# Kernel tuning notes

Hardware: AMD Instinct MI355X
Metric: run time of the kernel (lower is better)

Reference implementation:

```python
import jax, jax.numpy as jnp
import numpy as np

B, T, DM, H, D = 2, 2048, 1024, 16, 64
SCALE = D ** -0.5


def setup_inputs() -> dict:
    key = jax.random.key(0)
    ks = jax.random.split(key, 7)
    std = DM ** -0.5
    inp = {
        "x": jax.random.normal(ks[0], (B, T, DM), dtype=jnp.float32),
        "Wq_re": jax.random.normal(ks[1], (DM, H * D), dtype=jnp.float32) * std,
        "Wq_im": jax.random.normal(ks[2], (DM, H * D), dtype=jnp.float32) * std,
        "Wk_re": jax.random.normal(ks[3], (DM, H * D), dtype=jnp.float32) * std,
        "Wk_im": jax.random.normal(ks[4], (DM, H * D), dtype=jnp.float32) * std,
        "Wv": jax.random.normal(ks[5], (DM, H * D), dtype=jnp.float32) * std,
        "Wo": jax.random.normal(ks[6], (H * D, DM), dtype=jnp.float32) * std,
    }
    # standard RoPE angle cache: theta[t, d] = t * 10000^(-d/D)
    inv_freq = 1.0 / (10000.0 ** (np.arange(D, dtype=np.float32) / D))
    ang = np.arange(T, dtype=np.float32)[:, None] * inv_freq[None, :]
    inp["cos"] = jnp.asarray(np.cos(ang))
    inp["sin"] = jnp.asarray(np.sin(ang))
    return inp


def _split(x, W):
    # [B,T,DM] @ [DM,H*D] -> [B,H,T,D]
    return (x @ W).reshape(B, T, H, D).transpose(0, 2, 1, 3)


def reference(x, Wq_re, Wq_im, Wk_re, Wk_im, Wv, Wo, cos, sin):
    q_re, q_im = _split(x, Wq_re), _split(x, Wq_im)
    k_re, k_im = _split(x, Wk_re), _split(x, Wk_im)

    # complex RoPE: rotate (re, im) by e^{i*theta}; cos/sin broadcast over b,h
    c = cos[None, None]  # [1,1,T,D]
    s = sin[None, None]
    q_re, q_im = q_re * c - q_im * s, q_re * s + q_im * c
    k_re, k_im = k_re * c - k_im * s, k_re * s + k_im * c

    # Hermitian inner product real part: q_re.k_re + q_im.k_im
    scores = (jnp.einsum("bhqd,bhkd->bhqk", q_re, k_re)
              + jnp.einsum("bhqd,bhkd->bhqk", q_im, k_im)) * SCALE

    causal = jnp.tril(jnp.ones((T, T), dtype=bool))
    scores = jnp.where(causal[None, None], scores, -jnp.inf)
    weights = jax.nn.softmax(scores, axis=-1)

    v = _split(x, Wv)
    out = jnp.einsum("bhqk,bhkd->bhqd", weights, v)  # [B,H,T,D]
    out = out.transpose(0, 2, 1, 3).reshape(B, T, H * D)
    return out @ Wo
```

## Files before the change

kernel.cpp:

```cpp
#include <hip/hip_runtime.h>
#include <math.h>

#define SCALE_ 0.125f

typedef _Float16 half_t;
typedef __attribute__((ext_vector_type(8))) _Float16 f16x8;
typedef __attribute__((ext_vector_type(4))) _Float16 f16x4;
typedef __attribute__((ext_vector_type(4))) float f32x4;

#define AS1 __attribute__((address_space(1)))
#define AS3 __attribute__((address_space(3)))

__device__ __forceinline__ f32x4 mfma16(f16x8 a, f16x8 b, f32x4 c) {
  return __builtin_amdgcn_mfma_f32_16x16x32_f16(a, b, c, 0, 0, 0);
}
__device__ __forceinline__ void gload16(const void* g, void* l) {
  __builtin_amdgcn_global_load_lds((const AS1 void*)g, (AS3 void*)l, 16, 0, 0);
}
__device__ __forceinline__ void split2(float f, half_t* h, half_t* l) {
  half_t hh = (half_t)f;
  *h = hh;
  *l = (half_t)(f - (float)hh);
}

__global__ __launch_bounds__(256) void convw_kernel(
    const float* __restrict__ W0, const float* __restrict__ W1,
    const float* __restrict__ W2, const float* __restrict__ W3,
    const float* __restrict__ W4, const float* __restrict__ W5,
    half_t* __restrict__ wh, half_t* __restrict__ wl)
{
  const int z = blockIdx.z;
  const float* W = (z == 0) ? W0 : (z == 1) ? W1 : (z == 2) ? W2
                  : (z == 3) ? W3 : (z == 4) ? W4 : W5;
  half_t* outh = wh + z * 1048576;
  half_t* outl = wl + z * 1048576;
  const int n0 = blockIdx.x * 32, k0 = blockIdx.y * 32;
  const int t = threadIdx.x, r = t >> 3, c4 = (t & 7) * 4;
  __shared__ float lds[32][33];
  float4 v = *(const float4*)&W[(k0 + r) * 1024 + n0 + c4];
  lds[r][c4 + 0] = v.x; lds[r][c4 + 1] = v.y;
  lds[r][c4 + 2] = v.z; lds[r][c4 + 3] = v.w;
  __syncthreads();
  f16x4 oh, ol;
#pragma unroll
  for (int j = 0; j < 4; ++j) {
    const float f = lds[c4 + j][r];
    half_t hv, lv; split2(f, &hv, &lv);
    oh[j] = hv; ol[j] = lv;
  }
  *(f16x4*)&outh[(n0 + r) * 1024 + k0 + c4] = oh;
  *(f16x4*)&outl[(n0 + r) * 1024 + k0 + c4] = ol;
}

__global__ __launch_bounds__(256) void convx_kernel(
    const float* __restrict__ x, half_t* __restrict__ xh, half_t* __restrict__ xl)
{
  const int i = (blockIdx.x * 256 + threadIdx.x) * 4;
  float4 v = *(const float4*)&x[i];
  float vv[4] = {v.x, v.y, v.z, v.w};
  f16x4 oh, ol;
#pragma unroll
  for (int j = 0; j < 4; ++j) {
    half_t hv, lv; split2(vv[j], &hv, &lv);
    oh[j] = hv; ol[j] = lv;
  }
  *(f16x4*)&xh[i] = oh;
  *(f16x4*)&xl[i] = ol;
}

__global__ __launch_bounds__(256) void gemm_kernel(
    const half_t* __restrict__ Agh, const half_t* __restrict__ Agl,
    const half_t* __restrict__ wh, const half_t* __restrict__ wl,
    half_t* __restrict__ qth, half_t* __restrict__ qtl,
    half_t* __restrict__ kth, half_t* __restrict__ ktl,
    half_t* __restrict__ vTh, half_t* __restrict__ vTl,
    float* __restrict__ outp, int final_mode)
{
  __shared__ half_t Ash[4096], Asl[4096], Bsh[4096], Bsl[4096];
  const int z = blockIdx.z;
  const int widx = final_mode ? 5 : z;
  const half_t* Bth = wh + widx * 1048576;
  const half_t* Btl = wl + widx * 1048576;

  const int n0 = blockIdx.x * 128, m0 = blockIdx.y * 128;
  const int tid = threadIdx.x, lane = tid & 63, wid = tid >> 6;
  const int wr = wid >> 1, wc = wid & 1, l15 = lane & 15, l4 = lane >> 4;

  f32x4 acc[4][4];
#pragma unroll
  for (int i = 0; i < 4; ++i)
#pragma unroll
    for (int j = 0; j < 4; ++j) acc[i][j] = (f32x4){0.f, 0.f, 0.f, 0.f};

  const int s0 = wid * 64 + lane, s1 = s0 + 256;
  const int r0 = s0 >> 2, c0 = (s0 & 3) * 8;
  const int r1 = s1 >> 2, c1 = (s1 & 3) * 8;
  half_t* Ah0 = Ash + wid * 512;        half_t* Ah1 = Ash + 2048 + wid * 512;
  half_t* Al0 = Asl + wid * 512;        half_t* Al1 = Asl + 2048 + wid * 512;
  half_t* Bh0 = Bsh + wid * 512;        half_t* Bh1 = Bsh + 2048 + wid * 512;
  half_t* Bl0 = Bsl + wid * 512;        half_t* Bl1 = Bsl + 2048 + wid * 512;

  for (int k0 = 0; k0 < 1024; k0 += 32) {
    __syncthreads();
    gload16(Agh + (m0 + r0) * 1024 + k0 + c0, Ah0);
    gload16(Agh + (m0 + r1) * 1024 + k0 + c1, Ah1);
    gload16(Agl + (m0 + r0) * 1024 + k0 + c0, Al0);
    gload16(Agl + (m0 + r1) * 1024 + k0 + c1, Al1);
    gload16(Bth + (n0 + r0) * 1024 + k0 + c0, Bh0);
    gload16(Bth + (n0 + r1) * 1024 + k0 + c1, Bh1);
    gload16(Btl + (n0 + r0) * 1024 + k0 + c0, Bl0);
    gload16(Btl + (n0 + r1) * 1024 + k0 + c1, Bl1);
    __syncthreads();
    f16x8 ah[4], al[4], bh[4], bl[4];
#pragma unroll
    for (int i = 0; i < 4; ++i) {
      const int ro = (wr * 64 + i * 16 + l15) * 32 + l4 * 8;
      ah[i] = *(const f16x8*)&Ash[ro];
      al[i] = *(const f16x8*)&Asl[ro];
    }
#pragma unroll
    for (int j = 0; j < 4; ++j) {
      const int ro = (wc * 64 + j * 16 + l15) * 32 + l4 * 8;
      bh[j] = *(const f16x8*)&Bsh[ro];
      bl[j] = *(const f16x8*)&Bsl[ro];
    }
#pragma unroll
    for (int i = 0; i < 4; ++i)
#pragma unroll
      for (int j = 0; j < 4; ++j) {
        acc[i][j] = mfma16(ah[i], bh[j], acc[i][j]);
        acc[i][j] = mfma16(ah[i], bl[j], acc[i][j]);
        acc[i][j] = mfma16(al[i], bh[j], acc[i][j]);
      }
  }

#pragma unroll
  for (int i = 0; i < 4; ++i) {
    const int mb = m0 + wr * 64 + i * 16 + l4 * 4;
#pragma unroll
    for (int j = 0; j < 4; ++j) {
      const int n = n0 + wc * 64 + j * 16 + l15;
      if (final_mode) {
#pragma unroll
        for (int r = 0; r < 4; ++r) outp[(mb + r) * 1024 + n] = acc[i][j][r];
      } else if (z < 4) {
        half_t* dh = (z < 2) ? qth : kth;
        half_t* dl = (z < 2) ? qtl : ktl;
        const int colr = (n >> 6) * 128 + (n & 63) + ((z & 1) ? 64 : 0);
#pragma unroll
        for (int r = 0; r < 4; ++r) {
          half_t hv, lv; split2(acc[i][j][r], &hv, &lv);
          dh[(mb + r) * 2048 + colr] = hv;
          dl[(mb + r) * 2048 + colr] = lv;
        }
      } else {
        const int hh = n >> 6, d = n & 63;
        const int bq = mb >> 11, t = mb & 2047;
        f16x4 vh4, vl4;
#pragma unroll
        for (int r = 0; r < 4; ++r) {
          half_t hv, lv; split2(acc[i][j][r], &hv, &lv);
          vh4[r] = hv; vl4[r] = lv;
        }
        const int off = ((bq * 16 + hh) * 64 + d) * 2048 + t;
        *(f16x4*)&vTh[off] = vh4;
        *(f16x4*)&vTl[off] = vl4;
      }
    }
  }
}

__global__ __launch_bounds__(256) void rope_kernel(
    const half_t* __restrict__ qth, const half_t* __restrict__ qtl,
    const half_t* __restrict__ kth, const half_t* __restrict__ ktl,
    const float* __restrict__ cosb, const float* __restrict__ sinb,
    half_t* __restrict__ qbh, half_t* __restrict__ qbl,
    half_t* __restrict__ kbh, half_t* __restrict__ kbl)
{
  const int z = blockIdx.y;
  const int g = blockIdx.x * 4 + (threadIdx.x >> 6);
  const int d = threadIdx.x & 63;
  const int m = g >> 4, h = g & 15;
  const int b = m >> 11, t = m & 2047;
  const half_t* sh = (z ? kth : qth) + m * 2048 + h * 128;
  const half_t* sl = (z ? ktl : qtl) + m * 2048 + h * 128;
  const float re = (float)sh[d] + (float)sl[d];
  const float im = (float)sh[64 + d] + (float)sl[64 + d];
  const float c = cosb[t * 64 + d], s = sinb[t * 64 + d];
  float rer = re * c - im * s;
  float imr = re * s + im * c;
  if (z == 0) { rer *= SCALE_; imr *= SCALE_; }
  half_t* dh = (z ? kbh : qbh) + ((b * 16 + h) * 2048 + t) * 128;
  half_t* dl = (z ? kbl : qbl) + ((b * 16 + h) * 2048 + t) * 128;
  half_t hv, lv;
  split2(rer, &hv, &lv); dh[d] = hv;      dl[d] = lv;
  split2(imr, &hv, &lv); dh[64 + d] = hv; dl[64 + d] = lv;
}

__global__ __launch_bounds__(512) void attn_kernel(
    const half_t* __restrict__ qbh, const half_t* __restrict__ qbl,
    const half_t* __restrict__ kbh, const half_t* __restrict__ kbl,
    const half_t* __restrict__ vTh, const half_t* __restrict__ vTl,
    half_t* __restrict__ abh, half_t* __restrict__ abl)
{
  const int i = blockIdx.x;
  const int bh = i & 31;
  const int idx = (i >> 5) & 7;
  const int qt = (i < 256) ? (15 - idx) : idx;
  const int b = bh >> 4, h = bh & 15;
  const int tid = threadIdx.x, lane = tid & 63, w = tid >> 6;
  const int l15 = lane & 15, l4 = lane >> 4;
  const int q0 = qt * 128;

  __shared__ half_t Kh[2][4096], Kl[2][4096];
  __shared__ half_t Vh[2][2048], Vl[2][2048];
  __shared__ half_t Ph[4096], Pl[4096];

  f16x8 qh[4], ql[4];
  {
    const int qoff = (bh * 2048 + q0 + w * 16 + l15) * 128;
#pragma unroll
    for (int c = 0; c < 4; ++c) {
      qh[c] = *(const f16x8*)(qbh + qoff + c * 32 + l4 * 8);
      ql[c] = *(const f16x8*)(qbl + qoff + c * 32 + l4 * 8);
    }
  }

  f32x4 o[4];
#pragma unroll
  for (int n = 0; n < 4; ++n) o[n] = (f32x4){0.f, 0.f, 0.f, 0.f};
  float mrow[4] = {-3e38f, -3e38f, -3e38f, -3e38f};
  float lrow[4] = {0.f, 0.f, 0.f, 0.f};

  const half_t* kh_p = kbh + (size_t)bh * 2048 * 128;
  const half_t* kl_p = kbl + (size_t)bh * 2048 * 128;
  const half_t* vh_p = vTh + (size_t)bh * 64 * 2048;
  const half_t* vl_p = vTl + (size_t)bh * 64 * 2048;

  const int krow = w * 4 + (lane >> 4);
  const int ks = lane & 15;
  const int kg = (ks & 8) | ((ks & 7) ^ (krow & 7));
  const int vrow = (w & 3) * 16 + (lane >> 2);
  const int vs = lane & 3;
  const int vg = vs ^ ((vrow >> 1) & 3);
  const bool vhi = (w < 4);

  const int nkt = 4 * (qt + 1);
  const int qminw = q0 + w * 16, qmaxw = qminw + 15;

  gload16(kh_p + (krow) * 128 + kg * 8, &Kh[0][w * 512]);
  gload16(kl_p + (krow) * 128 + kg * 8, &Kl[0][w * 512]);
  if (vhi) gload16(vh_p + vrow * 2048 + vg * 8, &Vh[0][(w & 3) * 512]);
  else     gload16(vl_p + vrow * 2048 + vg * 8, &Vl[0][(w & 3) * 512]);

  for (int kt = 0; kt < nkt; ++kt) {
    const int k0 = kt * 32;
    const int cb = kt & 1;
    __syncthreads();

    {
      const int k0n = (kt + 1 < nkt) ? k0 + 32 : 0;
      const int nb = cb ^ 1;
      gload16(kh_p + (k0n + krow) * 128 + kg * 8, &Kh[nb][w * 512]);
      gload16(kl_p + (k0n + krow) * 128 + kg * 8, &Kl[nb][w * 512]);
      if (vhi) gload16(vh_p + vrow * 2048 + k0n + vg * 8, &Vh[nb][(w & 3) * 512]);
      else     gload16(vl_p + vrow * 2048 + k0n + vg * 8, &Vl[nb][(w & 3) * 512]);
    }

    if (k0 > qmaxw) continue;

    f32x4 s[2];
    s[0] = (f32x4){0.f, 0.f, 0.f, 0.f};
    s[1] = (f32x4){0.f, 0.f, 0.f, 0.f};
#pragma unroll
    for (int c = 0; c < 4; ++c) {
#pragma unroll
      for (int n = 0; n < 2; ++n) {
        const int row = n * 16 + l15;
        const int co = c * 4 + l4;
        const int sr = (co & 8) | ((co & 7) ^ (row & 7));
        const f16x8 kfh = *(const f16x8*)&Kh[cb][row * 128 + sr * 8];
        const f16x8 kfl = *(const f16x8*)&Kl[cb][row * 128 + sr * 8];
        s[n] = mfma16(qh[c], kfh, s[n]);
        s[n] = mfma16(qh[c], kfl, s[n]);
        s[n] = mfma16(ql[c], kfh, s[n]);
      }
    }

    if (k0 + 31 > qminw) {
#pragma unroll
      for (int n = 0; n < 2; ++n)
#pragma unroll
        for (int r = 0; r < 4; ++r)
          if (k0 + n * 16 + l15 > qminw + l4 * 4 + r) s[n][r] = -3e38f;
    }

#pragma unroll
    for (int r = 0; r < 4; ++r) {
      float mx = fmaxf(s[0][r], s[1][r]);
      mx = fmaxf(mx, __shfl_xor(mx, 1));
      mx = fmaxf(mx, __shfl_xor(mx, 2));
      mx = fmaxf(mx, __shfl_xor(mx, 4));
      mx = fmaxf(mx, __shfl_xor(mx, 8));
      const float mnew = fmaxf(mrow[r], mx);
      const float alpha = __expf(mrow[r] - mnew);
      const float p0 = __expf(s[0][r] - mnew);
      const float p1 = __expf(s[1][r] - mnew);
      float rs = p0 + p1;
      rs += __shfl_xor(rs, 1);
      rs += __shfl_xor(rs, 2);
      rs += __shfl_xor(rs, 4);
      rs += __shfl_xor(rs, 8);
      lrow[r] = lrow[r] * alpha + rs;
      mrow[r] = mnew;
#pragma unroll
      for (int n = 0; n < 4; ++n) o[n][r] *= alpha;
      const int prow = w * 16 + l4 * 4 + r;
      const int psw = (prow >> 2) & 3;
      half_t hv, lv;
      split2(p0, &hv, &lv);
      {
        const int col = l15, sp = (col >> 3) ^ psw;
        Ph[prow * 32 + sp * 8 + (col & 7)] = hv;
        Pl[prow * 32 + sp * 8 + (col & 7)] = lv;
      }
      split2(p1, &hv, &lv);
      {
        const int col = 16 + l15, sp = (col >> 3) ^ psw;
        Ph[prow * 32 + sp * 8 + (col & 7)] = hv;
        Pl[prow * 32 + sp * 8 + (col & 7)] = lv;
      }
    }

    {
      const int prow = w * 16 + l15;
      const int spp = l4 ^ ((prow >> 2) & 3);
      const f16x8 pfh = *(const f16x8*)&Ph[prow * 32 + spp * 8];
      const f16x8 pfl = *(const f16x8*)&Pl[prow * 32 + spp * 8];
#pragma unroll
      for (int n = 0; n < 4; ++n) {
        const int vr = n * 16 + l15;
        const int sv = l4 ^ ((vr >> 1) & 3);
        const f16x8 vfh = *(const f16x8*)&Vh[cb][vr * 32 + sv * 8];
        const f16x8 vfl = *(const f16x8*)&Vl[cb][vr * 32 + sv * 8];
        o[n] = mfma16(pfh, vfh, o[n]);
        o[n] = mfma16(pfh, vfl, o[n]);
        o[n] = mfma16(pfl, vfh, o[n]);
      }
    }
  }

  const int mg = b * 2048 + q0 + w * 16 + l4 * 4;
#pragma unroll
  for (int r = 0; r < 4; ++r) {
    const float inv = 1.0f / lrow[r];
    const int m = mg + r;
#pragma unroll
    for (int n = 0; n < 4; ++n) {
      half_t hv, lv; split2(o[n][r] * inv, &hv, &lv);
      abh[m * 1024 + h * 64 + n * 16 + l15] = hv;
      abl[m * 1024 + h * 64 + n * 16 + l15] = lv;
    }
  }
}

extern "C" void kernel_launch(void* const* d_in, const int* in_sizes, int n_in,
                              void* d_out, int out_size, void* d_ws,
                              size_t ws_size, hipStream_t stream) {
  const float* x    = (const float*)d_in[0];
  const float* Wqre = (const float*)d_in[1];
  const float* Wqim = (const float*)d_in[2];
  const float* Wkre = (const float*)d_in[3];
  const float* Wkim = (const float*)d_in[4];
  const float* Wv   = (const float*)d_in[5];
  const float* Wo   = (const float*)d_in[6];
  const float* cosb = (const float*)d_in[7];
  const float* sinb = (const float*)d_in[8];

  char* w = (char*)d_ws;
  const size_t MB = (size_t)1 << 20;
  half_t* wh6 = (half_t*)(w + 0 * MB);
  half_t* wl6 = (half_t*)(w + 12 * MB);
  half_t* xh  = (half_t*)(w + 24 * MB);
  half_t* xl  = (half_t*)(w + 32 * MB);
  half_t* qth = (half_t*)(w + 40 * MB);
  half_t* qtl = (half_t*)(w + 56 * MB);
  half_t* kth = (half_t*)(w + 72 * MB);
  half_t* ktl = (half_t*)(w + 88 * MB);
  half_t* qbh = (half_t*)(w + 104 * MB);
  half_t* qbl = (half_t*)(w + 120 * MB);
  half_t* kbh = (half_t*)(w + 136 * MB);
  half_t* kbl = (half_t*)(w + 152 * MB);
  half_t* vTh = (half_t*)(w + 168 * MB);
  half_t* vTl = (half_t*)(w + 176 * MB);
  half_t* abh = (half_t*)(w + 40 * MB);
  half_t* abl = (half_t*)(w + 48 * MB);

  dim3 blk(256);
  convw_kernel<<<dim3(32, 32, 6), blk, 0, stream>>>(Wqre, Wqim, Wkre, Wkim, Wv,
                                                    Wo, wh6, wl6);
  convx_kernel<<<dim3(4096), blk, 0, stream>>>(x, xh, xl);
  gemm_kernel<<<dim3(8, 32, 5), blk, 0, stream>>>(xh, xl, wh6, wl6, qth, qtl,
                                                  kth, ktl, vTh, vTl, nullptr, 0);
  rope_kernel<<<dim3(16384, 2), blk, 0, stream>>>(qth, qtl, kth, ktl, cosb,
                                                  sinb, qbh, qbl, kbh, kbl);
  attn_kernel<<<dim3(512), dim3(512), 0, stream>>>(qbh, qbl, kbh, kbl, vTh,
                                                   vTl, abh, abl);
  gemm_kernel<<<dim3(8, 32, 1), blk, 0, stream>>>(abh, abl, wh6, wl6, nullptr,
                                                  nullptr, nullptr, nullptr,
                                                  nullptr, nullptr,
                                                  (float*)d_out, 1);
}
```

Measured before the change: 513.4 us.

## Fuse RoPE into paired re/im projection GEMM and drop V split-precision

Computes the real and imaginary Q/K projections in one block that shares the x tile, and applies RoPE and scaling in the epilogue, which removes the separate rope kernel and its intermediate buffers. The V projection and the P·V product in attention now use single fp16 operands instead of the hi/lo split, cutting three MFMAs to one and halving V/P memory traffic. The final projection moves into its own kernel. The trade-off is lower precision on the V path and higher register and LDS pressure in the paired GEMM.

```diff
diff --git a/kernel.cpp b/kernel.cpp
--- a/kernel.cpp
+++ b/kernel.cpp
@@ -68,139 +68,144 @@
   *(f16x4*)&xl[i] = ol;
 }
 
-__global__ __launch_bounds__(256) void gemm_kernel(
-    const half_t* __restrict__ Agh, const half_t* __restrict__ Agl,
+__global__ __launch_bounds__(256) void proj_pair_kernel(
+    const half_t* __restrict__ xh, const half_t* __restrict__ xl,
     const half_t* __restrict__ wh, const half_t* __restrict__ wl,
-    half_t* __restrict__ qth, half_t* __restrict__ qtl,
-    half_t* __restrict__ kth, half_t* __restrict__ ktl,
-    half_t* __restrict__ vTh, half_t* __restrict__ vTl,
-    float* __restrict__ outp, int final_mode)
+    const float* __restrict__ cosb, const float* __restrict__ sinb,
+    half_t* __restrict__ qbh, half_t* __restrict__ qbl,
+    half_t* __restrict__ kbh, half_t* __restrict__ kbl,
+    half_t* __restrict__ vTh)
 {
-  __shared__ half_t Ash[4096], Asl[4096], Bsh[4096], Bsl[4096];
+  __shared__ half_t Ash[4096], Asl[4096];
+  __shared__ half_t B0h[4096], B0l[4096], B1h[4096], B1l[4096];
   const int z = blockIdx.z;
-  const int widx = final_mode ? 5 : z;
-  const half_t* Bth = wh + widx * 1048576;
-  const half_t* Btl = wl + widx * 1048576;
+  const bool pair = (z < 2);
+  const half_t* BRh_g = wh + (pair ? (2 * z) : 4) * 1048576;
+  const half_t* BRl_g = wl + (pair ? (2 * z) : 4) * 1048576;
+  const half_t* BIh_g = wh + (2 * z + 1) * 1048576;
+  const half_t* BIl_g = wl + (2 * z + 1) * 1048576;
 
   const int n0 = blockIdx.x * 128, m0 = blockIdx.y * 128;
   const int tid = threadIdx.x, lane = tid & 63, wid = tid >> 6;
   const int wr = wid >> 1, wc = wid & 1, l15 = lane & 15, l4 = lane >> 4;
 
-  f32x4 acc[4][4];
+  f32x4 accR[4][4], accI[4][4];
 #pragma unroll
   for (int i = 0; i < 4; ++i)
 #pragma unroll
-    for (int j = 0; j < 4; ++j) acc[i][j] = (f32x4){0.f, 0.f, 0.f, 0.f};
+    for (int j = 0; j < 4; ++j) {
+      accR[i][j] = (f32x4){0.f, 0.f, 0.f, 0.f};
+      accI[i][j] = (f32x4){0.f, 0.f, 0.f, 0.f};
+    }
 
   const int s0 = wid * 64 + lane, s1 = s0 + 256;
   const int r0 = s0 >> 2, c0 = (s0 & 3) * 8;
   const int r1 = s1 >> 2, c1 = (s1 & 3) * 8;
-  half_t* Ah0 = Ash + wid * 512;        half_t* Ah1 = Ash + 2048 + wid * 512;
-  half_t* Al0 = Asl + wid * 512;        half_t* Al1 = Asl + 2048 + wid * 512;
-  half_t* Bh0 = Bsh + wid * 512;        half_t* Bh1 = Bsh + 2048 + wid * 512;
-  half_t* Bl0 = Bsl + wid * 512;        half_t* Bl1 = Bsl + 2048 + wid * 512;
+  half_t* A0 = Ash + wid * 512;   half_t* A1 = Ash + 2048 + wid * 512;
+  half_t* La0 = Asl + wid * 512;  half_t* La1 = Asl + 2048 + wid * 512;
+  half_t* R0 = B0h + wid * 512;   half_t* R1 = B0h + 2048 + wid * 512;
+  half_t* Lr0 = B0l + wid * 512;  half_t* Lr1 = B0l + 2048 + wid * 512;
+  half_t* I0 = B1h + wid * 512;   half_t* I1 = B1h + 2048 + wid * 512;
+  half_t* Li0 = B1l + wid * 512;  half_t* Li1 = B1l + 2048 + wid * 512;
 
   for (int k0 = 0; k0 < 1024; k0 += 32) {
     __syncthreads();
-    gload16(Agh + (m0 + r0) * 1024 + k0 + c0, Ah0);
-    gload16(Agh + (m0 + r1) * 1024 + k0 + c1, Ah1);
-    gload16(Agl + (m0 + r0) * 1024 + k0 + c0, Al0);
-    gload16(Agl + (m0 + r1) * 1024 + k0 + c1, Al1);
-    gload16(Bth + (n0 + r0) * 1024 + k0 + c0, Bh0);
-    gload16(Bth + (n0 + r1) * 1024 + k0 + c1, Bh1);
-    gload16(Btl + (n0 + r0) * 1024 + k0 + c0, Bl0);
-    gload16(Btl + (n0 + r1) * 1024 + k0 + c1, Bl1);
+    gload16(xh + (m0 + r0) * 1024 + k0 + c0, A0);
+    gload16(xh + (m0 + r1) * 1024 + k0 + c1, A1);
+    gload16(BRh_g + (n0 + r0) * 1024 + k0 + c0, R0);
+    gload16(BRh_g + (n0 + r1) * 1024 + k0 + c1, R1);
+    if (pair) {
+      gload16(xl + (m0 + r0) * 1024 + k0 + c0, La0);
+      gload16(xl + (m0 + r1) * 1024 + k0 + c1, La1);
+      gload16(BRl_g + (n0 + r0) * 1024 + k0 + c0, Lr0);
+      gload16(BRl_g + (n0 + r1) * 1024 + k0 + c1, Lr1);
+      gload16(BIh_g + (n0 + r0) * 1024 + k0 + c0, I0);
+      gload16(BIh_g + (n0 + r1) * 1024 + k0 + c1, I1);
+      gload16(BIl_g + (n0 + r0) * 1024 + k0 + c0, Li0);
+      gload16(BIl_g + (n0 + r1) * 1024 + k0 + c1, Li1);
+    }
     __syncthreads();
-    f16x8 ah[4], al[4], bh[4], bl[4];
+    f16x8 ah[4], al[4];
 #pragma unroll
     for (int i = 0; i < 4; ++i) {
       const int ro = (wr * 64 + i * 16 + l15) * 32 + l4 * 8;
       ah[i] = *(const f16x8*)&Ash[ro];
-      al[i] = *(const f16x8*)&Asl[ro];
+      if (pair) al[i] = *(const f16x8*)&Asl[ro];
     }
 #pragma unroll
     for (int j = 0; j < 4; ++j) {
       const int ro = (wc * 64 + j * 16 + l15) * 32 + l4 * 8;
-      bh[j] = *(const f16x8*)&Bsh[ro];
-      bl[j] = *(const f16x8*)&Bsl[ro];
-    }
-#pragma unroll
-    for (int i = 0; i < 4; ++i)
-#pragma unroll
-      for (int j = 0; j < 4; ++j) {
-        acc[i][j] = mfma16(ah[i], bh[j], acc[i][j]);
-        acc[i][j] = mfma16(ah[i], bl[j], acc[i][j]);
-        acc[i][j] = mfma16(al[i], bh[j], acc[i][j]);
-      }
-  }
-
-#pragma unroll
-  for (int i = 0; i < 4; ++i) {
-    const int mb = m0 + wr * 64 + i * 16 + l4 * 4;
-#pragma unroll
-    for (int j = 0; j < 4; ++j) {
-      const int n = n0 + wc * 64 + j * 16 + l15;
-      if (final_mode) {
-#pragma unroll
-        for (int r = 0; r < 4; ++r) outp[(mb + r) * 1024 + n] = acc[i][j][r];
-      } else if (z < 4) {
-        half_t* dh = (z < 2) ? qth : kth;
-        half_t* dl = (z < 2) ? qtl : ktl;
-        const int colr = (n >> 6) * 128 + (n & 63) + ((z & 1) ? 64 : 0);
-#pragma unroll
-        for (int r = 0; r < 4; ++r) {
-          half_t hv, lv; split2(acc[i][j][r], &hv, &lv);
-          dh[(mb + r) * 2048 + colr] = hv;
-          dl[(mb + r) * 2048 + colr] = lv;
+      const f16x8 bRh = *(const f16x8*)&B0h[ro];
+      if (pair) {
+        const f16x8 bRl = *(const f16x8*)&B0l[ro];
+        const f16x8 bIh = *(const f16x8*)&B1h[ro];
+        const f16x8 bIl = *(const f16x8*)&B1l[ro];
+#pragma unroll
+        for (int i = 0; i < 4; ++i) {
+          accR[i][j] = mfma16(ah[i], bRh, accR[i][j]);
+          accR[i][j] = mfma16(ah[i], bRl, accR[i][j]);
+          accR[i][j] = mfma16(al[i], bRh, accR[i][j]);
+          accI[i][j] = mfma16(ah[i], bIh, accI[i][j]);
+          accI[i][j] = mfma16(ah[i], bIl, accI[i][j]);
+          accI[i][j] = mfma16(al[i], bIh, accI[i][j]);
         }
       } else {
+#pragma unroll
+        for (int i = 0; i < 4; ++i)
+          accR[i][j] = mfma16(ah[i], bRh, accR[i][j]);
+      }
+    }
+  }
+
+  if (pair) {
+    half_t* dsth = z ? kbh : qbh;
+    half_t* dstl = z ? kbl : qbl;
+#pragma unroll
+    for (int i = 0; i < 4; ++i) {
+      const int mb = m0 + wr * 64 + i * 16 + l4 * 4;
+#pragma unroll
+      for (int j = 0; j < 4; ++j) {
+        const int n = n0 + wc * 64 + j * 16 + l15;
+        const int h = n >> 6, d = n & 63;
+#pragma unroll
+        for (int r = 0; r < 4; ++r) {
+          const int m = mb + r;
+          const int bq = m >> 11, t = m & 2047;
+          const float c = cosb[t * 64 + d], s = sinb[t * 64 + d];
+          const float re = accR[i][j][r], im = accI[i][j][r];
+          float rer = re * c - im * s;
+          float imr = re * s + im * c;
+          if (z == 0) { rer *= SCALE_; imr *= SCALE_; }
+          const size_t base = ((size_t)(bq * 16 + h) * 2048 + t) * 128;
+          half_t hv, lv;
+          split2(rer, &hv, &lv); dsth[base + d] = hv;      dstl[base + d] = lv;
+          split2(imr, &hv, &lv); dsth[base + 64 + d] = hv; dstl[base + 64 + d] = lv;
+        }
+      }
+    }
+  } else {
+#pragma unroll
+    for (int i = 0; i < 4; ++i) {
+      const int mb = m0 + wr * 64 + i * 16 + l4 * 4;
+      const int bq = mb >> 11, t = mb & 2047;
+#pragma unroll
+      for (int j = 0; j < 4; ++j) {
+        const int n = n0 + wc * 64 + j * 16 + l15;
         const int hh = n >> 6, d = n & 63;
-        const int bq = mb >> 11, t = mb & 2047;
-        f16x4 vh4, vl4;
-#pragma unroll
-        for (int r = 0; r < 4; ++r) {
-          half_t hv, lv; split2(acc[i][j][r], &hv, &lv);
-          vh4[r] = hv; vl4[r] = lv;
-        }
-        const int off = ((bq * 16 + hh) * 64 + d) * 2048 + t;
+        f16x4 vh4;
+#pragma unroll
+        for (int r = 0; r < 4; ++r) vh4[r] = (half_t)accR[i][j][r];
+        const size_t off = ((size_t)(bq * 16 + hh) * 64 + d) * 2048 + t;
         *(f16x4*)&vTh[off] = vh4;
-        *(f16x4*)&vTl[off] = vl4;
-      }
-    }
-  }
-}
-
-__global__ __launch_bounds__(256) void rope_kernel(
-    const half_t* __restrict__ qth, const half_t* __restrict__ qtl,
-    const half_t* __restrict__ kth, const half_t* __restrict__ ktl,
-    const float* __restrict__ cosb, const float* __restrict__ sinb,
-    half_t* __restrict__ qbh, half_t* __restrict__ qbl,
-    half_t* __restrict__ kbh, half_t* __restrict__ kbl)
-{
-  const int z = blockIdx.y;
-  const int g = blockIdx.x * 4 + (threadIdx.x >> 6);
-  const int d = threadIdx.x & 63;
-  const int m = g >> 4, h = g & 15;
-  const int b = m >> 11, t = m & 2047;
-  const half_t* sh = (z ? kth : qth) + m * 2048 + h * 128;
-  const half_t* sl = (z ? ktl : qtl) + m * 2048 + h * 128;
-  const float re = (float)sh[d] + (float)sl[d];
-  const float im = (float)sh[64 + d] + (float)sl[64 + d];
-  const float c = cosb[t * 64 + d], s = sinb[t * 64 + d];
-  float rer = re * c - im * s;
-  float imr = re * s + im * c;
-  if (z == 0) { rer *= SCALE_; imr *= SCALE_; }
-  half_t* dh = (z ? kbh : qbh) + ((b * 16 + h) * 2048 + t) * 128;
-  half_t* dl = (z ? kbl : qbl) + ((b * 16 + h) * 2048 + t) * 128;
-  half_t hv, lv;
-  split2(rer, &hv, &lv); dh[d] = hv;      dl[d] = lv;
-  split2(imr, &hv, &lv); dh[64 + d] = hv; dl[64 + d] = lv;
+      }
+    }
+  }
 }
 
 __global__ __launch_bounds__(512) void attn_kernel(
     const half_t* __restrict__ qbh, const half_t* __restrict__ qbl,
     const half_t* __restrict__ kbh, const half_t* __restrict__ kbl,
-    const half_t* __restrict__ vTh, const half_t* __restrict__ vTl,
+    const half_t* __restrict__ vTh,
     half_t* __restrict__ abh, half_t* __restrict__ abl)
 {
   const int i = blockIdx.x;
@@ -213,12 +218,12 @@
   const int q0 = qt * 128;
 
   __shared__ half_t Kh[2][4096], Kl[2][4096];
-  __shared__ half_t Vh[2][2048], Vl[2][2048];
-  __shared__ half_t Ph[4096], Pl[4096];
+  __shared__ half_t Vh[2][2048];
+  __shared__ half_t Ph[4096];
 
   f16x8 qh[4], ql[4];
   {
-    const int qoff = (bh * 2048 + q0 + w * 16 + l15) * 128;
+    const size_t qoff = ((size_t)bh * 2048 + q0 + w * 16 + l15) * 128;
 #pragma unroll
     for (int c = 0; c < 4; ++c) {
       qh[c] = *(const f16x8*)(qbh + qoff + c * 32 + l4 * 8);
@@ -235,7 +240,6 @@
   const half_t* kh_p = kbh + (size_t)bh * 2048 * 128;
   const half_t* kl_p = kbl + (size_t)bh * 2048 * 128;
   const half_t* vh_p = vTh + (size_t)bh * 64 * 2048;
-  const half_t* vl_p = vTl + (size_t)bh * 64 * 2048;
 
   const int krow = w * 4 + (lane >> 4);
   const int ks = lane & 15;
@@ -243,15 +247,13 @@
   const int vrow = (w & 3) * 16 + (lane >> 2);
   const int vs = lane & 3;
   const int vg = vs ^ ((vrow >> 1) & 3);
-  const bool vhi = (w < 4);
 
   const int nkt = 4 * (qt + 1);
   const int qminw = q0 + w * 16, qmaxw = qminw + 15;
 
-  gload16(kh_p + (krow) * 128 + kg * 8, &Kh[0][w * 512]);
-  gload16(kl_p + (krow) * 128 + kg * 8, &Kl[0][w * 512]);
-  if (vhi) gload16(vh_p + vrow * 2048 + vg * 8, &Vh[0][(w & 3) * 512]);
-  else     gload16(vl_p + vrow * 2048 + vg * 8, &Vl[0][(w & 3) * 512]);
+  gload16(kh_p + krow * 128 + kg * 8, &Kh[0][w * 512]);
+  gload16(kl_p + krow * 128 + kg * 8, &Kl[0][w * 512]);
+  if (w < 4) gload16(vh_p + vrow * 2048 + vg * 8, &Vh[0][(w & 3) * 512]);
 
   for (int kt = 0; kt < nkt; ++kt) {
     const int k0 = kt * 32;
@@ -263,8 +265,7 @@
       const int nb = cb ^ 1;
       gload16(kh_p + (k0n + krow) * 128 + kg * 8, &Kh[nb][w * 512]);
       gload16(kl_p + (k0n + krow) * 128 + kg * 8, &Kl[nb][w * 512]);
-      if (vhi) gload16(vh_p + vrow * 2048 + k0n + vg * 8, &Vh[nb][(w & 3) * 512]);
-      else     gload16(vl_p + vrow * 2048 + k0n + vg * 8, &Vl[nb][(w & 3) * 512]);
+      if (w < 4) gload16(vh_p + vrow * 2048 + k0n + vg * 8, &Vh[nb][(w & 3) * 512]);
     }
 
     if (k0 > qmaxw) continue;
@@ -317,18 +318,13 @@
       for (int n = 0; n < 4; ++n) o[n][r] *= alpha;
       const int prow = w * 16 + l4 * 4 + r;
       const int psw = (prow >> 2) & 3;
-      half_t hv, lv;
-      split2(p0, &hv, &lv);
       {
         const int col = l15, sp = (col >> 3) ^ psw;
-        Ph[prow * 32 + sp * 8 + (col & 7)] = hv;
-        Pl[prow * 32 + sp * 8 + (col & 7)] = lv;
-      }
-      split2(p1, &hv, &lv);
+        Ph[prow * 32 + sp * 8 + (col & 7)] = (half_t)p0;
+      }
       {
         const int col = 16 + l15, sp = (col >> 3) ^ psw;
-        Ph[prow * 32 + sp * 8 + (col & 7)] = hv;
-        Pl[prow * 32 + sp * 8 + (col & 7)] = lv;
+        Ph[prow * 32 + sp * 8 + (col & 7)] = (half_t)p1;
       }
     }
 
@@ -336,16 +332,12 @@
       const int prow = w * 16 + l15;
       const int spp = l4 ^ ((prow >> 2) & 3);
       const f16x8 pfh = *(const f16x8*)&Ph[prow * 32 + spp * 8];
-      const f16x8 pfl = *(const f16x8*)&Pl[prow * 32 + spp * 8];
 #pragma unroll
       for (int n = 0; n < 4; ++n) {
         const int vr = n * 16 + l15;
         const int sv = l4 ^ ((vr >> 1) & 3);
         const f16x8 vfh = *(const f16x8*)&Vh[cb][vr * 32 + sv * 8];
-        const f16x8 vfl = *(const f16x8*)&Vl[cb][vr * 32 + sv * 8];
         o[n] = mfma16(pfh, vfh, o[n]);
-        o[n] = mfma16(pfh, vfl, o[n]);
-        o[n] = mfma16(pfl, vfh, o[n]);
       }
     }
   }
@@ -360,6 +352,79 @@
       half_t hv, lv; split2(o[n][r] * inv, &hv, &lv);
       abh[m * 1024 + h * 64 + n * 16 + l15] = hv;
       abl[m * 1024 + h * 64 + n * 16 + l15] = lv;
+    }
+  }
+}
+
+__global__ __launch_bounds__(256) void outproj_kernel(
+    const half_t* __restrict__ Agh, const half_t* __restrict__ Agl,
+    const half_t* __restrict__ wh, const half_t* __restrict__ wl,
+    float* __restrict__ outp)
+{
+  __shared__ half_t Ash[4096], Asl[4096], Bsh[4096], Bsl[4096];
+  const half_t* Bth = wh + 5 * 1048576;
+  const half_t* Btl = wl + 5 * 1048576;
+
+  const int n0 = blockIdx.x * 128, m0 = blockIdx.y * 128;
+  const int tid = threadIdx.x, lane = tid & 63, wid = tid >> 6;
+  const int wr = wid >> 1, wc = wid & 1, l15 = lane & 15, l4 = lane >> 4;
+
+  f32x4 acc[4][4];
+#pragma unroll
+  for (int i = 0; i < 4; ++i)
+#pragma unroll
+    for (int j = 0; j < 4; ++j) acc[i][j] = (f32x4){0.f, 0.f, 0.f, 0.f};
+
+  const int s0 = wid * 64 + lane, s1 = s0 + 256;
+  const int r0 = s0 >> 2, c0 = (s0 & 3) * 8;
+  const int r1 = s1 >> 2, c1 = (s1 & 3) * 8;
+  half_t* Ah0 = Ash + wid * 512;        half_t* Ah1 = Ash + 2048 + wid * 512;
+  half_t* Al0 = Asl + wid * 512;        half_t* Al1 = Asl + 2048 + wid * 512;
+  half_t* Bh0 = Bsh + wid * 512;        half_t* Bh1 = Bsh + 2048 + wid * 512;
+  half_t* Bl0 = Bsl + wid * 512;        half_t* Bl1 = Bsl + 2048 + wid * 512;
+
+  for (int k0 = 0; k0 < 1024; k0 += 32) {
+    __syncthreads();
+    gload16(Agh + (m0 + r0) * 1024 + k0 + c0, Ah0);
+    gload16(Agh + (m0 + r1) * 1024 + k0 + c1, Ah1);
+    gload16(Agl + (m0 + r0) * 1024 + k0 + c0, Al0);
+    gload16(Agl + (m0 + r1) * 1024 + k0 + c1, Al1);
+    gload16(Bth + (n0 + r0) * 1024 + k0 + c0, Bh0);
+    gload16(Bth + (n0 + r1) * 1024 + k0 + c1, Bh1);
+    gload16(Btl + (n0 + r0) * 1024 + k0 + c0, Bl0);
+    gload16(Btl + (n0 + r1) * 1024 + k0 + c1, Bl1);
+    __syncthreads();
+    f16x8 ah[4], al[4], bh[4], bl[4];
+#pragma unroll
+    for (int i = 0; i < 4; ++i) {
+      const int ro = (wr * 64 + i * 16 + l15) * 32 + l4 * 8;
+      ah[i] = *(const f16x8*)&Ash[ro];
+      al[i] = *(const f16x8*)&Asl[ro];
+    }
+#pragma unroll
+    for (int j = 0; j < 4; ++j) {
+      const int ro = (wc * 64 + j * 16 + l15) * 32 + l4 * 8;
+      bh[j] = *(const f16x8*)&Bsh[ro];
+      bl[j] = *(const f16x8*)&Bsl[ro];
+    }
+#pragma unroll
+    for (int i = 0; i < 4; ++i)
+#pragma unroll
+      for (int j = 0; j < 4; ++j) {
+        acc[i][j] = mfma16(ah[i], bh[j], acc[i][j]);
+        acc[i][j] = mfma16(ah[i], bl[j], acc[i][j]);
+        acc[i][j] = mfma16(al[i], bh[j], acc[i][j]);
+      }
+  }
+
+#pragma unroll
+  for (int i = 0; i < 4; ++i) {
+    const int mb = m0 + wr * 64 + i * 16 + l4 * 4;
+#pragma unroll
+    for (int j = 0; j < 4; ++j) {
+      const int n = n0 + wc * 64 + j * 16 + l15;
+#pragma unroll
+      for (int r = 0; r < 4; ++r) outp[(mb + r) * 1024 + n] = acc[i][j][r];
     }
   }
 }
@@ -383,31 +448,22 @@
   half_t* wl6 = (half_t*)(w + 12 * MB);
   half_t* xh  = (half_t*)(w + 24 * MB);
   half_t* xl  = (half_t*)(w + 32 * MB);
-  half_t* qth = (half_t*)(w + 40 * MB);
-  half_t* qtl = (half_t*)(w + 56 * MB);
-  half_t* kth = (half_t*)(w + 72 * MB);
-  half_t* ktl = (half_t*)(w + 88 * MB);
-  half_t* qbh = (half_t*)(w + 104 * MB);
-  half_t* qbl = (half_t*)(w + 120 * MB);
-  half_t* kbh = (half_t*)(w + 136 * MB);
-  half_t* kbl = (half_t*)(w + 152 * MB);
-  half_t* vTh = (half_t*)(w + 168 * MB);
-  half_t* vTl = (half_t*)(w + 176 * MB);
-  half_t* abh = (half_t*)(w + 40 * MB);
-  half_t* abl = (half_t*)(w + 48 * MB);
+  half_t* qbh = (half_t*)(w + 40 * MB);
+  half_t* qbl = (half_t*)(w + 56 * MB);
+  half_t* kbh = (half_t*)(w + 72 * MB);
+  half_t* kbl = (half_t*)(w + 88 * MB);
+  half_t* vTh = (half_t*)(w + 104 * MB);
+  half_t* abh = (half_t*)(w + 112 * MB);
+  half_t* abl = (half_t*)(w + 120 * MB);
 
   dim3 blk(256);
   convw_kernel<<<dim3(32, 32, 6), blk, 0, stream>>>(Wqre, Wqim, Wkre, Wkim, Wv,
                                                     Wo, wh6, wl6);
   convx_kernel<<<dim3(4096), blk, 0, stream>>>(x, xh, xl);
-  gemm_kernel<<<dim3(8, 32, 5), blk, 0, stream>>>(xh, xl, wh6, wl6, qth, qtl,
-                                                  kth, ktl, vTh, vTl, nullptr, 0);
-  rope_kernel<<<dim3(16384, 2), blk, 0, stream>>>(qth, qtl, kth, ktl, cosb,
-                                                  sinb, qbh, qbl, kbh, kbl);
+  proj_pair_kernel<<<dim3(8, 32, 3), blk, 0, stream>>>(
+      xh, xl, wh6, wl6, cosb, sinb, qbh, qbl, kbh, kbl, vTh);
   attn_kernel<<<dim3(512), dim3(512), 0, stream>>>(qbh, qbl, kbh, kbl, vTh,
-                                                   vTl, abh, abl);
-  gemm_kernel<<<dim3(8, 32, 1), blk, 0, stream>>>(abh, abl, wh6, wl6, nullptr,
-                                                  nullptr, nullptr, nullptr,
-                                                  nullptr, nullptr,
-                                                  (float*)d_out, 1);
-}
+                                                   abh, abl);
+  outproj_kernel<<<dim3(8, 32), blk, 0, stream>>>(abh, abl, wh6, wl6,
+                                                  (float*)d_out);
+}
```

Result: faster. 476.3 us (-7.2%).
